# Performance work log

Hardware: AMD Instinct MI355X
Metric: run time of the kernel (lower is better)

## Reference

```python
import jax, jax.numpy as jnp
import numpy as np

M0 = 0.3  # DTM mass parameter (layer init m0)
LIMS = [[-1.0, 1.0], [-1.0, 1.0]]
BY = 0.025


def _make_grid(lims, by):
    # Exact replica of tf_gridBy (including row ordering via full transpose)
    axes = [np.arange(lo, hi + by, by, dtype=np.float32) for lo, hi in lims]
    mesh = np.stack(np.meshgrid(*axes, indexing='ij'), 0)   # [d, n1, n2]
    grid = np.transpose(mesh).reshape(-1, len(lims))        # [N, d]
    return jnp.asarray(grid)


def setup_inputs() -> dict:
    key = jax.random.key(0)
    k1, k2 = jax.random.split(key)
    B, M = 2, 2048
    inputs = jax.random.normal(k1, (B, M, 2), dtype=jnp.float32)
    weight = jax.random.uniform(k2, (B, M), dtype=jnp.float32)  # positive weights
    grid = _make_grid(LIMS, BY)  # [6561, 2]
    return {"inputs": inputs, "weight": weight, "grid": grid}


def reference(inputs, weight, grid):
    # inputs: [B, M, d], weight: [B, M], grid: [N, d] -> dtm: [B, N]
    # Uses k = M (full sorted neighbor list); identical math to the original
    # data-dependent k = max(searchsorted)+1 truncation, since searchsorted
    # selects the same prefix index either way.
    wB = M0 * jnp.sum(weight, -1, keepdims=True)            # [B, 1] weightBound

    # Brute-force euclidean cdist grid -> points (tf_knn, r=2)
    X2 = jnp.sum(inputs * inputs, -1)                        # [B, M]
    G2 = jnp.sum(grid * grid, -1)                            # [N]
    XG = jnp.einsum('bmd,nd->bnm', inputs, grid)             # [B, N, M]
    dist = jnp.sqrt(jnp.maximum(G2[None, :, None] + X2[:, None, :] - 2.0 * XG, 0.0))

    # Full ascending sort = top_k with k=M (knnDistance, knnIndex)
    idx = jnp.argsort(dist, axis=-1)                         # [B, N, M]
    dsort = jnp.take_along_axis(dist, idx, axis=-1)

    # gather weights by neighbor index, cumulative mass
    wTemp = jnp.take_along_axis(jnp.broadcast_to(weight[:, None, :], idx.shape), idx, axis=-1)
    wcum = jnp.cumsum(wTemp, -1)                             # [B, N, M]

    bound = wB[..., None]                                    # [B, 1, 1]
    # searchsorted(side='left') == count of entries strictly below bound
    kidx = jnp.sum(wcum < bound, -1)                         # [B, N]

    d2 = dsort * dsort
    cumD = jnp.cumsum(d2 * wTemp, -1)
    val = cumD + d2 * (bound - wcum)                         # [B, N, M]
    sel = jnp.take_along_axis(val, kidx[..., None], axis=-1)[..., 0]  # [B, N]
    return jnp.sqrt(sel / wB)
```

## Files before the change

kernel.cpp:

```cpp
#include <hip/hip_runtime.h>
#include <math.h>


#define M_POINTS 2048
#define PER_LANE 32
#define M0 0.3f

__device__ __forceinline__ float wave_reduce_sum(float v) {
    #pragma unroll
    for (int off = 1; off < 64; off <<= 1)
        v += __shfl_xor(v, off, 64);
    return v;
}

__global__ __launch_bounds__(256) void dtm_kernel(
    const float* __restrict__ inputs,
    const float* __restrict__ weight,
    const float* __restrict__ grid,
    float* __restrict__ out,
    int B, int N)
{
    const int lane = threadIdx.x & 63;
    const int gwave = blockIdx.x * (blockDim.x >> 6) + (threadIdx.x >> 6);
    if (gwave >= B * N) return;
    const int b = gwave / N;
    const int n = gwave - b * N;

    const float gx = grid[2 * n];
    const float gy = grid[2 * n + 1];

    const float* __restrict__ inb = inputs + (size_t)b * M_POINTS * 2;
    const float* __restrict__ wb  = weight + (size_t)b * M_POINTS;

    float d2[PER_LANE], w[PER_LANE];
    float wsum_local = 0.0f;
    #pragma unroll
    for (int j = 0; j < PER_LANE; ++j) {
        const int m = lane + 64 * j;
        const float2 xy = *reinterpret_cast<const float2*>(inb + 2 * m);
        const float wt = wb[m];
        const float dx = xy.x - gx;
        const float dy = xy.y - gy;
        d2[j] = fmaf(dx, dx, dy * dy);
        w[j]  = wt;
        wsum_local += wt;
    }
    const float bound = M0 * wave_reduce_sum(wsum_local);

    int lo = -1;
    int hi = 0x7F800000;
    #pragma unroll 1
    for (int it = 0; it < 31; ++it) {
        const int mid = lo + ((hi - lo) >> 1);
        const float midf = __int_as_float(mid);
        float c = 0.0f;
        #pragma unroll
        for (int j = 0; j < PER_LANE; ++j)
            c += (d2[j] <= midf) ? w[j] : 0.0f;
        c = wave_reduce_sum(c);
        if (c >= bound) hi = mid; else lo = mid;
    }
    const float r2 = __int_as_float(hi);

    float S = 0.0f, W = 0.0f;
    #pragma unroll
    for (int j = 0; j < PER_LANE; ++j) {
        if (d2[j] < r2) {
            S = fmaf(w[j], d2[j], S);
            W += w[j];
        }
    }
    S = wave_reduce_sum(S);
    W = wave_reduce_sum(W);

    const float margin = fmaxf(bound - W, 0.0f);
    const float val = fmaxf(fmaf(r2, margin, S), 0.0f);
    if (lane == 0) out[gwave] = sqrtf(val / bound);
}

extern "C" void kernel_launch(void* const* d_in, const int* in_sizes, int n_in,
                              void* d_out, int out_size, void* d_ws, size_t ws_size,
                              hipStream_t stream) {
    const float* inputs = (const float*)d_in[0];
    const float* weight = (const float*)d_in[1];
    const float* grid   = (const float*)d_in[2];
    float* out = (float*)d_out;

    const int N = in_sizes[2] / 2;
    const int B = out_size / N;

    const int total_waves = B * N;
    const int waves_per_block = 256 / 64;
    const int blocks = (total_waves + waves_per_block - 1) / waves_per_block;

    dtm_kernel<<<blocks, 256, 0, stream>>>(inputs, weight, grid, out, B, N);
}
```

Before: 129.2 us.

## Use value-range bisection with weight-gap exit and exact min-step finish

Replaces the fixed 31-step bisection over float bit patterns with a bisection over the actual distance range [0, max d2]. It stops early once the weight between the brackets falls below 0.75, then walks forward through the next distinct distances, one at a time, to land on the exact threshold. Input loads also become contiguous per-lane float4 loads instead of strided float2 loads. The aim is fewer wave-wide reduction iterations. The cost is a data-dependent loop count, possible float-precision differences at the bracket edges, and a per-lane layout that leaves global reads uncoalesced across the wave.

```diff
diff --git a/kernel.cpp b/kernel.cpp
--- a/kernel.cpp
+++ b/kernel.cpp
@@ -10,6 +10,18 @@
     #pragma unroll
     for (int off = 1; off < 64; off <<= 1)
         v += __shfl_xor(v, off, 64);
+    return v;
+}
+__device__ __forceinline__ float wave_reduce_max(float v) {
+    #pragma unroll
+    for (int off = 1; off < 64; off <<= 1)
+        v = fmaxf(v, __shfl_xor(v, off, 64));
+    return v;
+}
+__device__ __forceinline__ float wave_reduce_min(float v) {
+    #pragma unroll
+    for (int off = 1; off < 64; off <<= 1)
+        v = fminf(v, __shfl_xor(v, off, 64));
     return v;
 }
 
@@ -32,46 +44,68 @@
     const float* __restrict__ inb = inputs + (size_t)b * M_POINTS * 2;
     const float* __restrict__ wb  = weight + (size_t)b * M_POINTS;
 
+    const int base = lane * PER_LANE;
+    const float4* __restrict__ xyv = reinterpret_cast<const float4*>(inb + 2 * base);
+    const float4* __restrict__ wv  = reinterpret_cast<const float4*>(wb + base);
+
     float d2[PER_LANE], w[PER_LANE];
-    float wsum_local = 0.0f;
+    float wsum_local = 0.0f, vmax_local = 0.0f;
     #pragma unroll
-    for (int j = 0; j < PER_LANE; ++j) {
-        const int m = lane + 64 * j;
-        const float2 xy = *reinterpret_cast<const float2*>(inb + 2 * m);
-        const float wt = wb[m];
-        const float dx = xy.x - gx;
-        const float dy = xy.y - gy;
-        d2[j] = fmaf(dx, dx, dy * dy);
-        w[j]  = wt;
-        wsum_local += wt;
+    for (int q = 0; q < PER_LANE / 4; ++q) {
+        const float4 wq = wv[q];
+        const float4 a  = xyv[2 * q];
+        const float4 c4 = xyv[2 * q + 1];
+        float dx, dy;
+        dx = a.x  - gx; dy = a.y  - gy; d2[4*q+0] = fmaf(dx, dx, dy * dy);
+        dx = a.z  - gx; dy = a.w  - gy; d2[4*q+1] = fmaf(dx, dx, dy * dy);
+        dx = c4.x - gx; dy = c4.y - gy; d2[4*q+2] = fmaf(dx, dx, dy * dy);
+        dx = c4.z - gx; dy = c4.w - gy; d2[4*q+3] = fmaf(dx, dx, dy * dy);
+        w[4*q+0] = wq.x; w[4*q+1] = wq.y; w[4*q+2] = wq.z; w[4*q+3] = wq.w;
+        wsum_local += wq.x + wq.y + wq.z + wq.w;
+        vmax_local = fmaxf(vmax_local, fmaxf(fmaxf(d2[4*q+0], d2[4*q+1]),
+                                             fmaxf(d2[4*q+2], d2[4*q+3])));
     }
-    const float bound = M0 * wave_reduce_sum(wsum_local);
+    const float total = wave_reduce_sum(wsum_local);
+    const float bound = M0 * total;
 
-    int lo = -1;
-    int hi = 0x7F800000;
+    float vlo = -1.0f, wlo = 0.0f;
+    float vhi = wave_reduce_max(vmax_local), whi = total;
     #pragma unroll 1
-    for (int it = 0; it < 31; ++it) {
-        const int mid = lo + ((hi - lo) >> 1);
-        const float midf = __int_as_float(mid);
+    for (int it = 0; it < 48; ++it) {
+        if (whi - wlo <= 0.75f) break;
+        const float vmid = 0.5f * (vlo + vhi);
+        if (!(vmid > vlo && vmid < vhi)) break;
         float c = 0.0f;
         #pragma unroll
         for (int j = 0; j < PER_LANE; ++j)
-            c += (d2[j] <= midf) ? w[j] : 0.0f;
+            c += (d2[j] <= vmid) ? w[j] : 0.0f;
         c = wave_reduce_sum(c);
-        if (c >= bound) hi = mid; else lo = mid;
+        if (c >= bound) { vhi = vmid; whi = c; }
+        else            { vlo = vmid; wlo = c; }
     }
-    const float r2 = __int_as_float(hi);
 
-    float S = 0.0f, W = 0.0f;
+    float r2 = vhi, W = wlo;
+    #pragma unroll 1
+    for (int step = 0; step < 64; ++step) {
+        float m = __builtin_inff();
+        #pragma unroll
+        for (int j = 0; j < PER_LANE; ++j)
+            m = fminf(m, (d2[j] > vlo) ? d2[j] : __builtin_inff());
+        m = wave_reduce_min(m);
+        float c = 0.0f;
+        #pragma unroll
+        for (int j = 0; j < PER_LANE; ++j)
+            c += (d2[j] <= m) ? w[j] : 0.0f;
+        c = wave_reduce_sum(c);
+        if (c >= bound) { r2 = m; W = wlo; break; }
+        vlo = m; wlo = c;
+    }
+
+    float S = 0.0f;
     #pragma unroll
-    for (int j = 0; j < PER_LANE; ++j) {
-        if (d2[j] < r2) {
-            S = fmaf(w[j], d2[j], S);
-            W += w[j];
-        }
-    }
+    for (int j = 0; j < PER_LANE; ++j)
+        if (d2[j] < r2) S = fmaf(w[j], d2[j], S);
     S = wave_reduce_sum(S);
-    W = wave_reduce_sum(W);
 
     const float margin = fmaxf(bound - W, 0.0f);
     const float val = fmaxf(fmaf(r2, margin, S), 0.0f);
```

Result: no change. 128.2 us (-0.8%).
